# Optimization experiments

Hardware: AMD Instinct MI355X
Metric: run time of the kernel (lower is better)

## Reference

```python
import jax, jax.numpy as jnp
import numpy as np

B, N, HID, NHEADS, VOCAB = 8, 2048, 768, 4, 15
ALPHA = 0.2  # LeakyReLU negative slope
NEG = -9e15  # matches -9000000000000000.0 mask constant


def setup_inputs() -> dict:
    key = jax.random.key(0)
    ks = jax.random.split(key, 7)
    node_feats = jax.random.randint(ks[0], (B, N), 0, VOCAB, dtype=jnp.int32)
    adjs = jax.random.randint(ks[1], (B, N, N), 0, 2, dtype=jnp.int32)
    embed_table = jax.random.normal(ks[2], (VOCAB, HID), dtype=jnp.float32)
    W_heads = jax.random.normal(ks[3], (NHEADS, HID, HID), dtype=jnp.float32) * 0.05
    a_heads = jax.random.normal(ks[4], (NHEADS, 2 * HID, 1), dtype=jnp.float32) * 0.05
    W_out = jax.random.normal(ks[5], (NHEADS * HID, HID), dtype=jnp.float32) * 0.05
    a_out = jax.random.normal(ks[6], (2 * HID, 1), dtype=jnp.float32) * 0.05
    return {"node_feats": node_feats, "adjs": adjs, "embed_table": embed_table,
            "W_heads": W_heads, "a_heads": a_heads, "W_out": W_out, "a_out": a_out}


def gat_layer(h, adj, W, a, concat):
    # h: (B,N,Fin), adj: (B,N,N), W: (Fin,Fout), a: (2*Fout,1)
    Fout = W.shape[1]
    Wh = jnp.matmul(h, W)                      # (B,N,Fout)
    Wh1 = jnp.matmul(Wh, a[:Fout])             # (B,N,1)
    Wh2 = jnp.matmul(Wh, a[Fout:])             # (B,N,1)
    e = Wh1 + jnp.swapaxes(Wh2, 1, 2)          # (B,N,N)
    e = jax.nn.leaky_relu(e, negative_slope=ALPHA)
    e = jnp.where(adj > 0, e, NEG)
    att = jax.nn.softmax(e, axis=-1)           # (B,N,N)
    h_prime = jnp.matmul(att, Wh)              # (B,N,Fout)
    return jax.nn.elu(h_prime) if concat else h_prime


def reference(node_feats, adjs, embed_table, W_heads, a_heads, W_out, a_out):
    x = embed_table[node_feats]                # (B,N,HID)  (shape_enc treated as identity)
    # multi-head GAT, heads vmapped then concatenated along feature dim
    heads = jax.vmap(lambda W, a: gat_layer(x, adjs, W, a, concat=True))(W_heads, a_heads)
    x = jnp.concatenate(jnp.moveaxis(heads, 0, -2).reshape(B, N, 1, NHEADS * HID).squeeze(2)[None], axis=0)[0] if False else jnp.transpose(heads, (1, 2, 0, 3)).reshape(B, N, NHEADS * HID)
    x = jax.nn.elu(gat_layer(x, adjs, W_out, a_out, concat=False))  # (B,N,HID)
    # pooling_forward with all-ones mask -> masked mean over node dim
    sum_emb = jnp.sum(x, axis=1)               # (B,HID)
    denom = jnp.maximum(jnp.full_like(sum_emb, float(N)), 1e-9)
    return sum_emb / denom                     # (B,HID)
```

## Files before the change

kernel.cpp:

```cpp
#include <hip/hip_runtime.h>
#include <math.h>

#define BB 8
#define NN 2048
#define HID 768
#define NHEADS 4
#define VOCAB 15
#define ALPHA 0.2f
#define NEGV -9e15f
#define MTOT (BB * NN)

using short4v = __attribute__((ext_vector_type(4))) short;
using short8v = __attribute__((ext_vector_type(8))) short;
using f32x4 = __attribute__((ext_vector_type(4))) float;

__device__ __forceinline__ short f2bf(float f) {
  union { float f; unsigned u; } x;
  x.f = f;
  unsigned r = x.u + 0x7fffu + ((x.u >> 16) & 1u);
  return (short)(r >> 16);
}

__device__ __forceinline__ void cp16(const void* g, void* l) {
  __builtin_amdgcn_global_load_lds(
      (const __attribute__((address_space(1))) unsigned int*)g,
      (__attribute__((address_space(3))) unsigned int*)l, 16, 0, 0);
}

#define MEMFENCE asm volatile("" ::: "memory")
#define SBAR()                         \
  do {                                 \
    MEMFENCE;                          \
    __builtin_amdgcn_s_barrier();      \
    MEMFENCE;                          \
  } while (0)

#define PACK_B 8192
#define ZERO_B 308
#define NFM_B 64
#define TRAN_B 2304
#define TW_B 192
__global__ __launch_bounds__(256) void setup_kernel(
    const int* __restrict__ adj, unsigned long long* __restrict__ packed,
    float* __restrict__ zbase, const int* __restrict__ nf,
    unsigned long long* __restrict__ nfm, const float* __restrict__ W_out,
    short* __restrict__ Wt_o, const float* __restrict__ table,
    const float* __restrict__ W_heads, float* __restrict__ TWp) {
  const int bid = blockIdx.x;
  const int tid = threadIdx.x;
  if (bid < PACK_B) {
    __shared__ unsigned short us[256];
    long base = (long)bid * 4096;
    const int4* ap = (const int4*)(adj + base + tid * 16);
    unsigned nib16 = 0;
#pragma unroll
    for (int k = 0; k < 4; ++k) {
      int4 a = ap[k];
      unsigned nib = (a.x > 0 ? 1u : 0u) | (a.y > 0 ? 2u : 0u) |
                     (a.z > 0 ? 4u : 0u) | (a.w > 0 ? 8u : 0u);
      nib16 |= nib << (4 * k);
    }
    us[tid] = (unsigned short)nib16;
    __syncthreads();
    if (tid < 64) {
      unsigned long long w =
          (unsigned long long)us[4 * tid] |
          ((unsigned long long)us[4 * tid + 1] << 16) |
          ((unsigned long long)us[4 * tid + 2] << 32) |
          ((unsigned long long)us[4 * tid + 3] << 48);
      packed[(base >> 6) + tid] = w;
    }
  } else if (bid < PACK_B + ZERO_B) {
    zbase[(bid - PACK_B) * 256 + tid] = 0.f;
  } else if (bid < PACK_B + ZERO_B + NFM_B) {
    int r = bid - PACK_B - ZERO_B;
    int b = r >> 3, c = r & 7;
    int w = tid >> 6;
    int j = c * 256 + tid;
    int nfv = nf[b * NN + j];
#pragma unroll
    for (int v = 0; v < VOCAB; ++v) {
      unsigned long long m = __ballot(nfv == v);
      if ((tid & 63) == 0) nfm[((long)b * VOCAB + v) * 32 + c * 4 + w] = m;
    }
  } else if (bid < PACK_B + ZERO_B + NFM_B + TRAN_B) {
    __shared__ float t[32][33];
    int r2 = bid - PACK_B - ZERO_B - NFM_B;
    const int K = NHEADS * HID, N = HID;
    int k0 = (r2 % 96) * 32, n0 = (r2 / 96) * 32;
    int tx = tid & 31, ty = tid >> 5;
#pragma unroll
    for (int i = 0; i < 32; i += 8)
      t[ty + i][tx] = W_out[(long)(k0 + ty + i) * N + n0 + tx];
    __syncthreads();
#pragma unroll
    for (int i = 0; i < 32; i += 8)
      Wt_o[(long)(n0 + ty + i) * K + k0 + tx] = f2bf(t[tx][ty + i]);
  } else {
    __shared__ float tbl[VOCAB][48];
    int r3 = bid - PACK_B - ZERO_B - NFM_B - TRAN_B;
    const int cx = r3 % 12, ky = r3 / 12;
    const int c = cx * 256 + tid;
    const int h = (cx * 256) / HID;
    const int n = c - h * HID;
    const int k0 = ky * 48;
    for (int idx = tid; idx < VOCAB * 48; idx += 256)
      tbl[idx / 48][idx % 48] = table[(idx / 48) * HID + k0 + idx % 48];
    __syncthreads();
    float acc[VOCAB];
#pragma unroll
    for (int v = 0; v < VOCAB; ++v) acc[v] = 0.f;
    const float* wp = W_heads + (long)h * HID * HID + (long)k0 * HID + n;
#pragma unroll 8
    for (int kk = 0; kk < 48; ++kk) {
      float w = wp[(long)kk * HID];
#pragma unroll
      for (int v = 0; v < VOCAB; ++v) acc[v] = fmaf(tbl[v][kk], w, acc[v]);
    }
#pragma unroll
    for (int v = 0; v < VOCAB; ++v)
      TWp[((long)ky * VOCAB + v) * (NHEADS * HID) + c] = acc[v];
  }
}

__global__ __launch_bounds__(256) void tw_finish_kernel(
    const float* __restrict__ TWp, float* __restrict__ TW,
    const float* __restrict__ a_heads, float* __restrict__ TW1,
    float* __restrict__ TW2) {
  const int tid = threadIdx.x;
  const int c = blockIdx.x * 256 + tid;
  const int h = (blockIdx.x * 256) / HID;
  const int n = c - h * HID;
  const float a1 = a_heads[h * 2 * HID + n];
  const float a2 = a_heads[h * 2 * HID + HID + n];
  const int lane = tid & 63;
  const int wv = tid >> 6;
  __shared__ float red[4][2 * VOCAB];

  float s1[VOCAB], s2[VOCAB];
#pragma unroll
  for (int v = 0; v < VOCAB; ++v) {
    float s = 0.f;
#pragma unroll
    for (int ky = 0; ky < 16; ++ky)
      s += TWp[((long)ky * VOCAB + v) * (NHEADS * HID) + c];
    TW[v * (NHEADS * HID) + c] = s;
    s1[v] = s * a1;
    s2[v] = s * a2;
  }
#pragma unroll
  for (int off = 1; off < 64; off <<= 1)
#pragma unroll
    for (int v = 0; v < VOCAB; ++v) {
      s1[v] += __shfl_xor(s1[v], off);
      s2[v] += __shfl_xor(s2[v], off);
    }
  if (lane == 0) {
#pragma unroll
    for (int v = 0; v < VOCAB; ++v) {
      red[wv][v] = s1[v];
      red[wv][VOCAB + v] = s2[v];
    }
  }
  __syncthreads();
  if (tid < 2 * VOCAB) {
    float s = red[0][tid] + red[1][tid] + red[2][tid] + red[3][tid];
    float* dst = (tid < VOCAB) ? (TW1 + h * VOCAB + tid)
                               : (TW2 + h * VOCAB + tid - VOCAB);
    atomicAdd(dst, s);
  }
}

__global__ __launch_bounds__(256) void p16_kernel(
    const int* __restrict__ nf, const unsigned* __restrict__ padj32,
    const unsigned* __restrict__ nfm32, const float* __restrict__ TW1,
    const float* __restrict__ TW2, float* __restrict__ P16) {
  const int t = threadIdx.x;
  const int wv = t >> 6;
  const int lane = t & 63;
  const int rowm = blockIdx.x * 4 + wv;
  const int b = rowm >> 11;
  __shared__ float cnts[4][16];

  unsigned a = padj32[(long)rowm * 64 + lane];
  const unsigned* nb = nfm32 + (long)b * VOCAB * 64 + lane;
  int cnt[VOCAB];
#pragma unroll
  for (int v = 0; v < VOCAB; ++v) cnt[v] = __popc(a & nb[v * 64]);
#pragma unroll
  for (int off = 1; off < 64; off <<= 1)
#pragma unroll
    for (int v = 0; v < VOCAB; ++v) cnt[v] += __shfl_xor(cnt[v], off);
  int cntsum = 0;
#pragma unroll
  for (int v = 0; v < VOCAB; ++v) cntsum += cnt[v];
  const bool use_full = (cntsum == 0);
  if (use_full) {
#pragma unroll
    for (int v = 0; v < VOCAB; ++v) cnt[v] = __popc(nb[v * 64]);
#pragma unroll
    for (int off = 1; off < 64; off <<= 1)
#pragma unroll
      for (int v = 0; v < VOCAB; ++v) cnt[v] += __shfl_xor(cnt[v], off);
  }
  if (lane < 16) cnts[wv][lane] = (lane < VOCAB) ? (float)cnt[lane] : 0.f;
  __syncthreads();

  const int h = lane >> 4;
  const int v = lane & 15;
  const int nfi = nf[b * NN + (rowm & 2047)];
  float cvf = cnts[wv][v];
  bool valid = (v < VOCAB) && (cvf > 0.f);
  float logit = 0.f;
  if (!use_full) {
    float s = TW1[h * VOCAB + nfi] + ((v < VOCAB) ? TW2[h * VOCAB + v] : 0.f);
    logit = s > 0.f ? s : ALPHA * s;
  }
  float mv = valid ? logit : -INFINITY;
#pragma unroll
  for (int off = 1; off < 16; off <<= 1) mv = fmaxf(mv, __shfl_xor(mv, off));
  float pv = valid ? cvf * __expf(logit - mv) : 0.f;
  float sum = pv;
#pragma unroll
  for (int off = 1; off < 16; off <<= 1) sum += __shfl_xor(sum, off);
  if (v < VOCAB) P16[((long)h * 16384 + rowm) * 16 + v] = pv / sum;
}

__global__ __launch_bounds__(256) void hcat_expand(
    const float* __restrict__ TW, const float* __restrict__ P16,
    short* __restrict__ hcat) {
  __shared__ float pl[128 * 16];
  const int c0 = blockIdx.x * 128;
  const int r0 = blockIdx.y * 128;
  const int h = c0 / HID;
  const int t = threadIdx.x;
  for (int idx = t; idx < 128 * 16; idx += 256)
    pl[idx] = P16[((long)h * 16384 + r0 + (idx >> 4)) * 16 + (idx & 15)];
  const int clb = (t & 31) * 4;
  const int rlb = (t >> 5) * 16;
  float twc[VOCAB][4];
#pragma unroll
  for (int vv = 0; vv < VOCAB; ++vv) {
    float4 q = *(const float4*)(TW + (long)vv * (NHEADS * HID) + c0 + clb);
    twc[vv][0] = q.x; twc[vv][1] = q.y; twc[vv][2] = q.z; twc[vv][3] = q.w;
  }
  __syncthreads();
#pragma unroll 4
  for (int rr = 0; rr < 16; ++rr) {
    int rl = rlb + rr;
    const float* pr = pl + rl * 16;
    float4 p0 = *(const float4*)(pr);
    float4 p1 = *(const float4*)(pr + 4);
    float4 p2 = *(const float4*)(pr + 8);
    float4 p3 = *(const float4*)(pr + 12);
    float pv[VOCAB] = {p0.x, p0.y, p0.z, p0.w, p1.x, p1.y, p1.z, p1.w,
                       p2.x, p2.y, p2.z, p2.w, p3.x, p3.y, p3.z};
    short4v o;
#pragma unroll
    for (int cc = 0; cc < 4; ++cc) {
      float s = 0.f;
#pragma unroll
      for (int vv = 0; vv < VOCAB; ++vv) s = fmaf(pv[vv], twc[vv][cc], s);
      s = s > 0.f ? s : (__expf(s) - 1.f);
      o[cc] = f2bf(s);
    }
    *(short4v*)(hcat + (long)(r0 + rl) * (NHEADS * HID) + c0 + clb) = o;
  }
}

template <int MODE>
__device__ __forceinline__ void gemm_core(
    short (*As)[8192], short (*Bs)[24576],
    const short* __restrict__ A, const short* __restrict__ B,
    int K, int lda, int ldb, int m0, int n0, int z,
    float* __restrict__ Cf, short* __restrict__ Ct,
    const float* __restrict__ a_vec, float* __restrict__ Wh1g,
    float* __restrict__ Wh2g) {
  const int tid = threadIdx.x;
  const int lane = tid & 63;
  const int wid = tid >> 6;
  const int l15 = lane & 15;
  const int quad = lane >> 4;
  const int NT = K >> 6;
  const int cbase = (quad ^ (l15 & 7)) << 3;

  auto stageA = [&](int kt) {
    const short* src = A + (long)m0 * lda + kt * 64;
    short* dst = As[kt & 1];
#pragma unroll
    for (int it = 0; it < 2; ++it) {
      int lin = it * 512 + tid;
      int r = lin >> 3, s = lin & 7;
      cp16(src + (long)r * lda + ((s ^ (r & 7)) << 3), dst + lin * 8);
    }
  };
  auto stageB = [&](int kt) {
    const short* src = B + (long)n0 * ldb + kt * 64;
    short* dst = Bs[kt & 1];
#pragma unroll
    for (int it = 0; it < 6; ++it) {
      int lin = it * 512 + tid;
      int r = lin >> 3, s = lin & 7;
      cp16(src + (long)r * ldb + ((s ^ (r & 7)) << 3), dst + lin * 8);
    }
  };

  f32x4 acc[8][3];
#pragma unroll
  for (int i = 0; i < 8; ++i)
#pragma unroll
    for (int j = 0; j < 3; ++j) acc[i][j] = (f32x4){0.f, 0.f, 0.f, 0.f};

  stageA(0);
  stageB(0);
  asm volatile("s_waitcnt vmcnt(0)" ::: "memory");
  SBAR();

#pragma unroll 1
  for (int t = 0; t < NT; ++t) {
    const short* Ab = As[t & 1];
    const short* Bb = Bs[t & 1];
    short8v a[4][2], b[3][2];

    if (t + 1 < NT) { stageB(t + 1); stageA(t + 1); }
#pragma unroll
    for (int ii = 0; ii < 4; ++ii) {
      int ro = (ii * 16 + l15) * 64;
      a[ii][0] = *(const short8v*)(Ab + ro + cbase);
      a[ii][1] = *(const short8v*)(Ab + ro + (cbase ^ 32));
    }
#pragma unroll
    for (int nj = 0; nj < 3; ++nj) {
      int ro = (wid * 48 + nj * 16 + l15) * 64;
      b[nj][0] = *(const short8v*)(Bb + ro + cbase);
      b[nj][1] = *(const short8v*)(Bb + ro + (cbase ^ 32));
    }
    SBAR();
    asm volatile("s_waitcnt lgkmcnt(0)" ::: "memory");
    __builtin_amdgcn_sched_barrier(0);
    __builtin_amdgcn_s_setprio(1);
#pragma unroll
    for (int ii = 0; ii < 4; ++ii)
#pragma unroll
      for (int nj = 0; nj < 3; ++nj) {
        acc[ii][nj] = __builtin_amdgcn_mfma_f32_16x16x32_bf16(
            a[ii][0], b[nj][0], acc[ii][nj], 0, 0, 0);
        acc[ii][nj] = __builtin_amdgcn_mfma_f32_16x16x32_bf16(
            a[ii][1], b[nj][1], acc[ii][nj], 0, 0, 0);
      }
    __builtin_amdgcn_sched_barrier(0);
    __builtin_amdgcn_s_setprio(0);
    SBAR();

#pragma unroll
    for (int ii = 0; ii < 4; ++ii) {
      int ro = (64 + ii * 16 + l15) * 64;
      a[ii][0] = *(const short8v*)(Ab + ro + cbase);
      a[ii][1] = *(const short8v*)(Ab + ro + (cbase ^ 32));
    }
    SBAR();
    asm volatile("s_waitcnt lgkmcnt(0)" ::: "memory");
    __builtin_amdgcn_sched_barrier(0);
    __builtin_amdgcn_s_setprio(1);
#pragma unroll
    for (int ii = 0; ii < 4; ++ii)
#pragma unroll
      for (int nj = 0; nj < 3; ++nj) {
        acc[4 + ii][nj] = __builtin_amdgcn_mfma_f32_16x16x32_bf16(
            a[ii][0], b[nj][0], acc[4 + ii][nj], 0, 0, 0);
        acc[4 + ii][nj] = __builtin_amdgcn_mfma_f32_16x16x32_bf16(
            a[ii][1], b[nj][1], acc[4 + ii][nj], 0, 0, 0);
      }
    __builtin_amdgcn_sched_barrier(0);
    __builtin_amdgcn_s_setprio(0);
    if (t + 1 < NT) {
      asm volatile("s_waitcnt vmcnt(0)" ::: "memory");
    }
    SBAR();
  }

  if constexpr (MODE == 3) {
#pragma unroll
    for (int nj = 0; nj < 3; ++nj) {
      int col = n0 + wid * 48 + nj * 16 + l15;
      float s = 0.f;
#pragma unroll
      for (int mi = 0; mi < 8; ++mi)
#pragma unroll
        for (int reg = 0; reg < 4; ++reg) {
          float v = acc[mi][nj][reg];
          s += v > 0.f ? v : (__expf(v) - 1.f);
        }
      s += __shfl_xor(s, 16);
      s += __shfl_xor(s, 32);
      if (quad == 0) atomicAdd(Cf + (long)z * HID + col, s * (1.0f / NN));
    }
  } else {
    float a1v[3], a2v[3];
#pragma unroll
    for (int nj = 0; nj < 3; ++nj) {
      int colh = n0 + wid * 48 + nj * 16 + l15;
      a1v[nj] = a_vec[colh];
      a2v[nj] = a_vec[HID + colh];
    }
#pragma unroll
    for (int mi = 0; mi < 8; ++mi) {
      int rb = m0 + mi * 16 + quad * 4;
#pragma unroll
      for (int reg = 0; reg < 4; ++reg) {
        float s1 = 0.f, s2 = 0.f;
#pragma unroll
        for (int nj = 0; nj < 3; ++nj) {
          s1 = fmaf(acc[mi][nj][reg], a1v[nj], s1);
          s2 = fmaf(acc[mi][nj][reg], a2v[nj], s2);
        }
#pragma unroll
        for (int off = 1; off < 16; off <<= 1) {
          s1 += __shfl_xor(s1, off);
          s2 += __shfl_xor(s2, off);
        }
        if (l15 == 0) {
          atomicAdd(Wh1g + rb + reg, s1);
          atomicAdd(Wh2g + rb + reg, s2);
        }
      }
    }
    const int bb = m0 >> 11;
    const int ml0 = m0 & 2047;
#pragma unroll
    for (int mi = 0; mi < 8; ++mi) {
#pragma unroll
      for (int nj = 0; nj < 3; ++nj) {
        int colh = n0 + wid * 48 + nj * 16 + l15;
        short4v pk;
#pragma unroll
        for (int reg = 0; reg < 4; ++reg) pk[reg] = f2bf(acc[mi][nj][reg]);
        *(short4v*)(Ct + ((long)bb * HID + colh) * NN + ml0 + mi * 16 +
                    quad * 4) = pk;
      }
    }
  }
}

__global__ __launch_bounds__(512, 2) void gemm_proj(
    const short* __restrict__ Ahc, const short* __restrict__ Bw,
    short* __restrict__ Ct, const float* __restrict__ a_vec,
    float* __restrict__ Wh1g, float* __restrict__ Wh2g) {
  __shared__ short As[2][8192];
  __shared__ short Bs[2][24576];
  int bid = blockIdx.x;
  int work = (bid & 7) * 32 + (bid >> 3);
  int bx = work >> 7;
  int by = work & 127;
  gemm_core<0>(As, Bs, Ahc, Bw, NHEADS * HID, NHEADS * HID, NHEADS * HID,
               by * 128, bx * 384, 0, nullptr, Ct, a_vec, Wh1g, Wh2g);
}

__global__ __launch_bounds__(512, 2) void gemm_attn(
    const short* __restrict__ att, const short* __restrict__ WhT,
    float* __restrict__ Cf) {
  __shared__ short As[2][8192];
  __shared__ short Bs[2][24576];
  int bid = blockIdx.x;
  int work = (bid & 7) * 32 + (bid >> 3);
  int z = work >> 5;
  int rem = work & 31;
  int bx = rem >> 4;
  int by = rem & 15;
  gemm_core<3>(As, Bs, att + (long)z * NN * NN, WhT + (long)z * HID * NN,
               NN, NN, NN, by * 128, bx * 384, z, Cf, nullptr, nullptr,
               nullptr, nullptr);
}

__global__ __launch_bounds__(256) void attn_softmax_kernel(
    const float* __restrict__ Wh1, const float* __restrict__ Wh2,
    const unsigned long long* __restrict__ packed, short* __restrict__ att,
    float* __restrict__ zA, int zn) {
  const int bid = blockIdx.x;
  const int t = threadIdx.x;
  if (bid < zn) zA[bid * 256 + t] = 0.f;
  const int b = bid >> 8;
  const int row0 = bid * 8;
  const int lane = t & 63;
  const int wv = t >> 6;
  const float* wh2b = Wh2 + b * NN;

  float4 wa = ((const float4*)(wh2b + t * 8))[0];
  float4 wb = ((const float4*)(wh2b + t * 8))[1];
  float w[8] = {wa.x, wa.y, wa.z, wa.w, wb.x, wb.y, wb.z, wb.w};

  __shared__ float redm[4], reds[4];
#pragma unroll 1
  for (int r = 0; r < 8; ++r) {
    const int row = row0 + r;
    unsigned m8 = ((const unsigned char*)(packed + (long)row * 32))[t];
    float wh1 = Wh1[row];
    float v[8];
    float lmax = -INFINITY;
#pragma unroll
    for (int k = 0; k < 8; ++k) {
      float s = wh1 + w[k];
      s = s > 0.f ? s : ALPHA * s;
      s = ((m8 >> k) & 1u) ? s : NEGV;
      v[k] = s;
      lmax = fmaxf(lmax, s);
    }
#pragma unroll
    for (int off = 32; off > 0; off >>= 1)
      lmax = fmaxf(lmax, __shfl_xor(lmax, off));
    if (lane == 0) redm[wv] = lmax;
    __syncthreads();
    float m = fmaxf(fmaxf(redm[0], redm[1]), fmaxf(redm[2], redm[3]));

    float lsum = 0.f;
#pragma unroll
    for (int k = 0; k < 8; ++k) {
      float p = __expf(v[k] - m);
      v[k] = p;
      lsum += p;
    }
#pragma unroll
    for (int off = 32; off > 0; off >>= 1) lsum += __shfl_xor(lsum, off);
    if (lane == 0) reds[wv] = lsum;
    __syncthreads();
    float inv = 1.f / (reds[0] + reds[1] + reds[2] + reds[3]);

    short8v o;
#pragma unroll
    for (int k = 0; k < 8; ++k) o[k] = f2bf(v[k] * inv);
    *(short8v*)(att + (long)row * NN + t * 8) = o;
  }
}

extern "C" void kernel_launch(void* const* d_in, const int* in_sizes, int n_in,
                              void* d_out, int out_size, void* d_ws,
                              size_t ws_size, hipStream_t stream) {
  const int* node_feats = (const int*)d_in[0];
  const int* adjs = (const int*)d_in[1];
  const float* embed_table = (const float*)d_in[2];
  const float* W_heads = (const float*)d_in[3];
  const float* a_heads = (const float*)d_in[4];
  const float* W_out = (const float*)d_in[5];
  const float* a_out = (const float*)d_in[6];
  float* out = (float*)d_out;

  char* p = (char*)d_ws;
  short* Wt_o = (short*)p;  p += (size_t)HID * (NHEADS * HID) * 2;
  short* Wh_t = (short*)p;  p += (size_t)BB * HID * NN * 2;
  short* att2 = (short*)p;  p += (size_t)BB * NN * NN * 2;
  short* hcat = (short*)p;  p += (size_t)MTOT * NHEADS * HID * 2;
  unsigned long long* padj = (unsigned long long*)p;
  p += (size_t)BB * NN * NN / 8;
  float* P16 = (float*)p;   p += (size_t)NHEADS * 16384 * 16 * 4;
  float* Wh1 = (float*)p;   p += (size_t)16384 * 4;
  float* Wh2 = (float*)p;   p += (size_t)16384 * 4;
  float* TW1 = (float*)p;   p += (size_t)64 * 4;
  float* TW2 = (float*)p;   p += (size_t)64 * 4;
  p += (size_t)(ZERO_B * 256 - 2 * 16384 - 128) * 4;
  float* TWp = (float*)p;   p += (size_t)16 * VOCAB * NHEADS * HID * 4;
  float* TW = (float*)p;    p += (size_t)VOCAB * NHEADS * HID * 4;
  unsigned long long* nfm = (unsigned long long*)p;
  p += (size_t)BB * VOCAB * 32 * 8;
  if ((size_t)(p - (char*)d_ws) > ws_size) return;

  setup_kernel<<<PACK_B + ZERO_B + NFM_B + TRAN_B + TW_B, 256, 0, stream>>>(
      adjs, padj, Wh1, node_feats, nfm, W_out, Wt_o, embed_table, W_heads,
      TWp);

  tw_finish_kernel<<<12, 256, 0, stream>>>(TWp, TW, a_heads, TW1, TW2);
  p16_kernel<<<16384 / 4, 256, 0, stream>>>(
      node_feats, (const unsigned*)padj, (const unsigned*)nfm, TW1, TW2, P16);
  hcat_expand<<<dim3(24, 128), 256, 0, stream>>>(TW, P16, hcat);

  gemm_proj<<<256, 512, 0, stream>>>(hcat, Wt_o, Wh_t, a_out, Wh1, Wh2);
  attn_softmax_kernel<<<MTOT / 8, 256, 0, stream>>>(Wh1, Wh2, padj, att2, out,
                                                    24);
  gemm_attn<<<256, 512, 0, stream>>>(att2, Wh_t, out);
}
```

Measured before the change: 469.2 us.

## Software-pipeline LDS fragment reads with MFMA using double-buffered B registers

```diff
diff --git a/kernel.cpp b/kernel.cpp
--- a/kernel.cpp
+++ b/kernel.cpp
@@ -305,78 +305,99 @@
     }
   };
 
+  short8v alo[4][2], ahi[4][2], bA[3][2], bB[3][2];
   f32x4 acc[8][3];
 #pragma unroll
   for (int i = 0; i < 8; ++i)
 #pragma unroll
     for (int j = 0; j < 3; ++j) acc[i][j] = (f32x4){0.f, 0.f, 0.f, 0.f};
+
+  auto readALO = [&](const short* Ab) {
+#pragma unroll
+    for (int ii = 0; ii < 4; ++ii) {
+      int ro = (ii * 16 + l15) * 64;
+      alo[ii][0] = *(const short8v*)(Ab + ro + cbase);
+      alo[ii][1] = *(const short8v*)(Ab + ro + (cbase ^ 32));
+    }
+  };
+  auto readAHI = [&](const short* Ab) {
+#pragma unroll
+    for (int ii = 0; ii < 4; ++ii) {
+      int ro = (64 + ii * 16 + l15) * 64;
+      ahi[ii][0] = *(const short8v*)(Ab + ro + cbase);
+      ahi[ii][1] = *(const short8v*)(Ab + ro + (cbase ^ 32));
+    }
+  };
+  auto readB = [&](const short* Bb, short8v (&bb)[3][2]) {
+#pragma unroll
+    for (int nj = 0; nj < 3; ++nj) {
+      int ro = (wid * 48 + nj * 16 + l15) * 64;
+      bb[nj][0] = *(const short8v*)(Bb + ro + cbase);
+      bb[nj][1] = *(const short8v*)(Bb + ro + (cbase ^ 32));
+    }
+  };
+  auto mfmaLO = [&](short8v (&bb)[3][2]) {
+#pragma unroll
+    for (int ii = 0; ii < 4; ++ii)
+#pragma unroll
+      for (int nj = 0; nj < 3; ++nj) {
+        acc[ii][nj] = __builtin_amdgcn_mfma_f32_16x16x32_bf16(
+            alo[ii][0], bb[nj][0], acc[ii][nj], 0, 0, 0);
+        acc[ii][nj] = __builtin_amdgcn_mfma_f32_16x16x32_bf16(
+            alo[ii][1], bb[nj][1], acc[ii][nj], 0, 0, 0);
+      }
+  };
+  auto mfmaHI = [&](short8v (&bb)[3][2]) {
+#pragma unroll
+    for (int ii = 0; ii < 4; ++ii)
+#pragma unroll
+      for (int nj = 0; nj < 3; ++nj) {
+        acc[4 + ii][nj] = __builtin_amdgcn_mfma_f32_16x16x32_bf16(
+            ahi[ii][0], bb[nj][0], acc[4 + ii][nj], 0, 0, 0);
+        acc[4 + ii][nj] = __builtin_amdgcn_mfma_f32_16x16x32_bf16(
+            ahi[ii][1], bb[nj][1], acc[4 + ii][nj], 0, 0, 0);
+      }
+  };
+
+  auto tileStep = [&](int t, short8v (&bcur)[3][2], short8v (&bnxt)[3][2]) {
+    const int p = t & 1;
+    if (t + 1 < NT) { stageB(t + 1); stageA(t + 1); }
+    readAHI(As[p]);
+    asm volatile("s_waitcnt lgkmcnt(8)" ::: "memory");
+    __builtin_amdgcn_sched_barrier(0);
+    __builtin_amdgcn_s_setprio(1);
+    mfmaLO(bcur);
+    __builtin_amdgcn_sched_barrier(0);
+    __builtin_amdgcn_s_setprio(0);
+    if (t + 1 < NT) {
+      asm volatile("s_waitcnt vmcnt(0)" ::: "memory");
+      SBAR();
+      readALO(As[(t + 1) & 1]);
+      readB(Bs[(t + 1) & 1], bnxt);
+      asm volatile("s_waitcnt lgkmcnt(14)" ::: "memory");
+    } else {
+      asm volatile("s_waitcnt lgkmcnt(0)" ::: "memory");
+      SBAR();
+    }
+    __builtin_amdgcn_sched_barrier(0);
+    __builtin_amdgcn_s_setprio(1);
+    mfmaHI(bcur);
+    __builtin_amdgcn_sched_barrier(0);
+    __builtin_amdgcn_s_setprio(0);
+    SBAR();
+  };
 
   stageA(0);
   stageB(0);
   asm volatile("s_waitcnt vmcnt(0)" ::: "memory");
   SBAR();
+  readALO(As[0]);
+  readB(Bs[0], bA);
 
 #pragma unroll 1
-  for (int t = 0; t < NT; ++t) {
-    const short* Ab = As[t & 1];
-    const short* Bb = Bs[t & 1];
-    short8v a[4][2], b[3][2];
-
-    if (t + 1 < NT) { stageB(t + 1); stageA(t + 1); }
-#pragma unroll
-    for (int ii = 0; ii < 4; ++ii) {
-      int ro = (ii * 16 + l15) * 64;
-      a[ii][0] = *(const short8v*)(Ab + ro + cbase);
-      a[ii][1] = *(const short8v*)(Ab + ro + (cbase ^ 32));
-    }
-#pragma unroll
-    for (int nj = 0; nj < 3; ++nj) {
-      int ro = (wid * 48 + nj * 16 + l15) * 64;
-      b[nj][0] = *(const short8v*)(Bb + ro + cbase);
-      b[nj][1] = *(const short8v*)(Bb + ro + (cbase ^ 32));
-    }
-    SBAR();
-    asm volatile("s_waitcnt lgkmcnt(0)" ::: "memory");
-    __builtin_amdgcn_sched_barrier(0);
-    __builtin_amdgcn_s_setprio(1);
-#pragma unroll
-    for (int ii = 0; ii < 4; ++ii)
-#pragma unroll
-      for (int nj = 0; nj < 3; ++nj) {
-        acc[ii][nj] = __builtin_amdgcn_mfma_f32_16x16x32_bf16(
-            a[ii][0], b[nj][0], acc[ii][nj], 0, 0, 0);
-        acc[ii][nj] = __builtin_amdgcn_mfma_f32_16x16x32_bf16(
-            a[ii][1], b[nj][1], acc[ii][nj], 0, 0, 0);
-      }
-    __builtin_amdgcn_sched_barrier(0);
-    __builtin_amdgcn_s_setprio(0);
-    SBAR();
-
-#pragma unroll
-    for (int ii = 0; ii < 4; ++ii) {
-      int ro = (64 + ii * 16 + l15) * 64;
-      a[ii][0] = *(const short8v*)(Ab + ro + cbase);
-      a[ii][1] = *(const short8v*)(Ab + ro + (cbase ^ 32));
-    }
-    SBAR();
-    asm volatile("s_waitcnt lgkmcnt(0)" ::: "memory");
-    __builtin_amdgcn_sched_barrier(0);
-    __builtin_amdgcn_s_setprio(1);
-#pragma unroll
-    for (int ii = 0; ii < 4; ++ii)
-#pragma unroll
-      for (int nj = 0; nj < 3; ++nj) {
-        acc[4 + ii][nj] = __builtin_amdgcn_mfma_f32_16x16x32_bf16(
-            a[ii][0], b[nj][0], acc[4 + ii][nj], 0, 0, 0);
-        acc[4 + ii][nj] = __builtin_amdgcn_mfma_f32_16x16x32_bf16(
-            a[ii][1], b[nj][1], acc[4 + ii][nj], 0, 0, 0);
-      }
-    __builtin_amdgcn_sched_barrier(0);
-    __builtin_amdgcn_s_setprio(0);
-    if (t + 1 < NT) {
-      asm volatile("s_waitcnt vmcnt(0)" ::: "memory");
-    }
-    SBAR();
+  for (int t = 0; t < NT; t += 2) {
+    tileStep(t, bA, bB);
+    tileStep(t + 1, bB, bA);
   }
 
   if constexpr (MODE == 3) {
```

Measured after the change: 487.1 us. 1.04x slower.
